# Optimization experiments

Hardware: AMD Instinct MI355X
Metric: run time of the kernel (lower is better)

Reference implementation:

```python
import jax, jax.numpy as jnp
import numpy as np

DIM = 768; DEPTH = 8; HEADS = 12; DH = 64; DFF = 2048
SOFTCLAMP = 50.0; TIME_EVERY = 4
B, T, S = 2, 32, 256
EPS = 1e-6


def rmsnorm(x, w):
    return x * jax.lax.rsqrt(jnp.mean(x * x, axis=-1, keepdims=True) + EPS) * w


def l2norm(x):
    n = jnp.sqrt(jnp.sum(x * x, axis=-1, keepdims=True))
    return x / jnp.maximum(n, 1e-12)


def make_rotary(n):
    inv = 1.0 / (10000.0 ** (jnp.arange(0, DH, 2, dtype=jnp.float32) / DH))
    f = jnp.arange(n, dtype=jnp.float32)[:, None] * inv[None, :]
    return jnp.concatenate([f, f], axis=-1)  # (n, DH)


def apply_rot(rot, x):
    # x: (B', H, n, DH), rot: (n, DH)
    x1, x2 = jnp.split(x, 2, axis=-1)
    return x * jnp.cos(rot) + jnp.concatenate([-x2, x1], axis=-1) * jnp.sin(rot)


def attn_block(x, rv, nw, wq, wk, wv, wo, wg, wmix, bm, kgam, rot, causal):
    # x: (B', n, DIM); rv: (B', H, n, DH) value-residual
    Bp, n, _ = x.shape
    tn = rmsnorm(x, nw)
    q = (tn @ wq).reshape(Bp, n, HEADS, DH).transpose(0, 2, 1, 3)
    k = (tn @ wk).reshape(Bp, n, HEADS, DH).transpose(0, 2, 1, 3)
    v = (tn @ wv).reshape(Bp, n, HEADS, DH).transpose(0, 2, 1, 3)
    # learned value-residual lerp: v <- v + mix * (rv - v)
    mix = jax.nn.sigmoid(tn @ wmix + bm).transpose(0, 2, 1)[..., None]
    v = v + mix * (rv - v)
    # MultiHeadRMSNorm on keys: l2norm * (gamma+1) * sqrt(DH)
    k = l2norm(k) * ((kgam + 1.0) * (DH ** 0.5))[:, None, :]
    if rot is not None:
        q = apply_rot(rot, q)
        k = apply_rot(rot, k)
    sim = jnp.einsum('bhid,bhjd->bhij', q, k) * (DH ** -0.5)
    sim = jnp.tanh(sim / SOFTCLAMP) * SOFTCLAMP
    if causal:
        cm = jnp.triu(jnp.ones((n, n), dtype=bool), 1)
        sim = jnp.where(cm, -jnp.finfo(sim.dtype).max, sim)
    attn = jax.nn.softmax(sim, axis=-1)
    o = jnp.einsum('bhij,bhjd->bhid', attn, v)
    gates = jax.nn.sigmoid(tn @ wg).transpose(0, 2, 1)[..., None]
    o = o * gates
    o = o.transpose(0, 2, 1, 3).reshape(Bp, n, HEADS * DH)
    return o @ wo


def ff_block(x, nw, win, bi, wout, bo):
    tn = rmsnorm(x, nw)
    h = tn @ win + bi
    a, g = jnp.split(h, 2, axis=-1)
    return (a * jax.nn.gelu(g, approximate=False)) @ wout + bo


def setup_inputs() -> dict:
    key = jax.random.key(0)
    ks = jax.random.split(key, 16)
    def rn(k, shape, scale=0.02):
        return jax.random.normal(k, shape, dtype=jnp.float32) * scale
    return {
        'tokens': jax.random.normal(ks[0], (B, T, S, DIM), dtype=jnp.float32),
        'attn_norm_w': jnp.ones((DEPTH, DIM), jnp.float32),
        'Wq': rn(ks[1], (DEPTH, DIM, HEADS * DH)),
        'Wk': rn(ks[2], (DEPTH, DIM, HEADS * DH)),
        'Wv': rn(ks[3], (DEPTH, DIM, HEADS * DH)),
        'Wo': rn(ks[4], (DEPTH, HEADS * DH, DIM)),
        'Wg': rn(ks[5], (DEPTH, DIM, HEADS)),
        'Wmix': rn(ks[6], (DEPTH, DIM, HEADS)),
        'bmix': jnp.zeros((DEPTH, HEADS), jnp.float32),
        'k_gamma': rn(ks[7], (DEPTH, HEADS, DH)),
        'ff_norm_w': jnp.ones((DEPTH, DIM), jnp.float32),
        'Win': rn(ks[8], (DEPTH, DIM, 2 * DFF)),
        'b_in': jnp.zeros((DEPTH, 2 * DFF), jnp.float32),
        'Wout': rn(ks[9], (DEPTH, DFF, DIM)),
        'b_out': jnp.zeros((DEPTH, DIM), jnp.float32),
        'vr_norm_w': jnp.ones((DIM,), jnp.float32),
        'vr_W': rn(ks[10], (DIM, HEADS * DH)),
        'final_norm_w': jnp.ones((DIM,), jnp.float32),
    }


def reference(tokens, attn_norm_w, Wq, Wk, Wv, Wo, Wg, Wmix, bmix, k_gamma,
              ff_norm_w, Win, b_in, Wout, b_out, vr_norm_w, vr_W, final_norm_w):
    b, t, s, d = tokens.shape
    # value residuals computed once from the input tokens
    rv = (rmsnorm(tokens, vr_norm_w) @ vr_W).reshape(b, t, s, HEADS, DH)
    rot = make_rotary(t)
    x = tokens
    for i in range(DEPTH):
        is_time = ((i + 1) % TIME_EVERY == 0)
        if is_time:
            xa = x.transpose(0, 2, 1, 3).reshape(b * s, t, d)
            rva = rv.transpose(0, 2, 3, 1, 4).reshape(b * s, HEADS, t, DH)
            o = attn_block(xa, rva, attn_norm_w[i], Wq[i], Wk[i], Wv[i], Wo[i],
                           Wg[i], Wmix[i], bmix[i], k_gamma[i], rot, True)
            o = o.reshape(b, s, t, d).transpose(0, 2, 1, 3)
        else:
            xa = x.reshape(b * t, s, d)
            rva = rv.transpose(0, 1, 3, 2, 4).reshape(b * t, HEADS, s, DH)
            o = attn_block(xa, rva, attn_norm_w[i], Wq[i], Wk[i], Wv[i], Wo[i],
                           Wg[i], Wmix[i], bmix[i], k_gamma[i], None, False)
            o = o.reshape(b, t, s, d)
        x = x + o
        x = x + ff_block(x, ff_norm_w[i], Win[i], b_in[i], Wout[i], b_out[i])
    return rmsnorm(x, final_norm_w)
```

## Files before the change

kernel.cpp:

```cpp
#include <hip/hip_runtime.h>
#include <cmath>

#define DIM 768
#define DEPTH 8
#define HEADS 12
#define DH 64
#define DFF 2048
#define NTOK 16384
#define BB 2
#define TT 32
#define SS 256
#define LDQ 2304

typedef __attribute__((ext_vector_type(8))) short short8;
typedef __attribute__((ext_vector_type(4))) float f32x4;

__device__ __forceinline__ float sigmoidf_(float x) { return 1.0f / (1.0f + __expf(-x)); }
__device__ __forceinline__ float geluf_(float x) {
  return 0.5f * x * (1.0f + erff(x * 0.70710678118654752f));
}
__device__ __forceinline__ unsigned short f2bf(float x) {
  union { float f; unsigned int u; } a; a.f = x;
  unsigned int r = a.u + 0x7fff + ((a.u >> 16) & 1);
  return (unsigned short)(r >> 16);
}
__device__ __forceinline__ float bf2f(unsigned short h) {
  union { unsigned int u; float f; } a; a.u = ((unsigned int)h) << 16;
  return a.f;
}
__device__ __forceinline__ void load_lds16(const void* g, void* l) {
  __builtin_amdgcn_global_load_lds(
      (const __attribute__((address_space(1))) unsigned int*)g,
      (__attribute__((address_space(3))) unsigned int*)l, 16, 0, 0);
}
__device__ __forceinline__ float softclamp_exp(float sv) {
  float a = exp2f(sv * 0.057707802f);
  float rc = __builtin_amdgcn_rcpf(a + 1.0f);
  return exp2f(fmaf(-144.26950408f, rc, 72.13475204f));
}

template<int BF>
__global__ __launch_bounds__(256) void rmsnorm_kernel(
    const float* __restrict__ x, const float* __restrict__ w, void* __restrict__ outp)
{
  int row = blockIdx.x;
  int tid = threadIdx.x;
  const float* xr = x + (size_t)row * DIM;
  float v0 = xr[tid], v1 = xr[tid + 256], v2 = xr[tid + 512];
  float ss = v0 * v0 + v1 * v1 + v2 * v2;
  #pragma unroll
  for (int off = 32; off; off >>= 1) ss += __shfl_xor(ss, off);
  __shared__ float sred[4];
  if ((tid & 63) == 0) sred[tid >> 6] = ss;
  __syncthreads();
  float tot = sred[0] + sred[1] + sred[2] + sred[3];
  float r = rsqrtf(tot * (1.0f / DIM) + 1e-6f);
  if (BF) {
    unsigned short* orow = (unsigned short*)outp + (size_t)row * DIM;
    orow[tid]       = f2bf(v0 * r * w[tid]);
    orow[tid + 256] = f2bf(v1 * r * w[tid + 256]);
    orow[tid + 512] = f2bf(v2 * r * w[tid + 512]);
  } else {
    float* orow = (float*)outp + (size_t)row * DIM;
    orow[tid]       = v0 * r * w[tid];
    orow[tid + 256] = v1 * r * w[tid + 256];
    orow[tid + 512] = v2 * r * w[tid + 512];
  }
}

__global__ __launch_bounds__(256) void w_to_bt(
    const float* __restrict__ W, unsigned short* __restrict__ WT, int K, int N)
{
  __shared__ float t[32][33];
  int n0 = blockIdx.x * 32, k0 = blockIdx.y * 32;
  int c = threadIdx.x & 31, r8 = threadIdx.x >> 5;
  #pragma unroll
  for (int rr = r8; rr < 32; rr += 8)
    t[rr][c] = W[(size_t)(k0 + rr) * N + n0 + c];
  __syncthreads();
  #pragma unroll
  for (int rn = r8; rn < 32; rn += 8)
    WT[(size_t)(n0 + rn) * K + k0 + c] = f2bf(t[c][rn]);
}

__global__ __launch_bounds__(256) void w_convert_layer(
    const float* __restrict__ Wq, const float* __restrict__ Wk,
    const float* __restrict__ Wv, const float* __restrict__ Wo,
    const float* __restrict__ Win, const float* __restrict__ Wout,
    unsigned short* __restrict__ wqkvT, unsigned short* __restrict__ woT,
    unsigned short* __restrict__ winT, unsigned short* __restrict__ woutT)
{
  __shared__ float tle[32][33];
  int t = blockIdx.x;
  const float* W; unsigned short* WT; int K, N, n0, k0, glu = 0;
  if (t < 1728) {
    int rg = t / 576, tt = t - rg * 576;
    W = (rg == 0) ? Wq : (rg == 1) ? Wk : Wv;
    WT = wqkvT + (size_t)rg * 768 * 768;
    K = 768; N = 768; n0 = (tt % 24) * 32; k0 = (tt / 24) * 32;
  } else if (t < 2304) {
    int tt = t - 1728; W = Wo; WT = woT;
    K = 768; N = 768; n0 = (tt % 24) * 32; k0 = (tt / 24) * 32;
  } else if (t < 5376) {
    int tt = t - 2304; W = Win; WT = winT;
    K = 768; N = 4096; n0 = (tt % 128) * 32; k0 = (tt / 128) * 32; glu = 1;
  } else {
    int tt = t - 5376; W = Wout; WT = woutT;
    K = 2048; N = 768; n0 = (tt % 24) * 32; k0 = (tt / 24) * 32;
  }
  int c = threadIdx.x & 31, r8 = threadIdx.x >> 5;
  int col = n0 + c;
  int scol = col;
  if (glu) {
    int b = col >> 5, rr2 = col & 31;
    scol = (rr2 < 16) ? (b * 16 + rr2) : (2048 + b * 16 + rr2 - 16);
  }
  for (int rr = r8; rr < 32; rr += 8)
    tle[rr][c] = W[(size_t)(k0 + rr) * N + scol];
  __syncthreads();
  for (int rn = r8; rn < 32; rn += 8)
    WT[(size_t)(n0 + rn) * K + k0 + c] = f2bf(tle[c][rn]);
}

template<int MODE>
__global__ __launch_bounds__(256) void gemm_bf16(
    const unsigned short* __restrict__ A, const unsigned short* __restrict__ BT,
    float* __restrict__ Cf, unsigned short* __restrict__ Hg,
    const float* __restrict__ bias, int M, int N, int K)
{
  __shared__ unsigned short As[128 * 32];
  __shared__ unsigned short Bs[128 * 32];
  const int tid = threadIdx.x;
  const int wave = tid >> 6;
  const int lane = tid & 63;
  const int bm = blockIdx.y * 128;
  const int bn = blockIdx.x * 128;
  const int wm = (wave & 1) * 64;
  const int wn = (wave >> 1) * 64;

  f32x4 acc[4][4];
  #pragma unroll
  for (int i = 0; i < 4; ++i)
    #pragma unroll
    for (int j = 0; j < 4; ++j) acc[i][j] = (f32x4){0.f, 0.f, 0.f, 0.f};

  const int srow = wave * 32 + (lane >> 2);
  const int skoff = (lane & 3) * 8;
  const unsigned short* gA = A + (size_t)(bm + srow) * K + skoff;
  const unsigned short* gB = BT + (size_t)(bn + srow) * K + skoff;
  unsigned short* lA = &As[(wave * 32) * 32];
  unsigned short* lB = &Bs[(wave * 32) * 32];

  const int fr = lane & 15;
  const int fq = (lane >> 4) * 8;

  for (int k0 = 0; k0 < K; k0 += 32) {
    load_lds16(gA + k0, lA);
    load_lds16(gA + k0 + 16 * K, lA + 16 * 32);
    load_lds16(gB + k0, lB);
    load_lds16(gB + k0 + 16 * K, lB + 16 * 32);
    __syncthreads();
    short8 a[4], b[4];
    #pragma unroll
    for (int i = 0; i < 4; ++i)
      a[i] = *(const short8*)&As[(wm + 16 * i + fr) * 32 + fq];
    #pragma unroll
    for (int j = 0; j < 4; ++j)
      b[j] = *(const short8*)&Bs[(wn + 16 * j + fr) * 32 + fq];
    #pragma unroll
    for (int i = 0; i < 4; ++i)
      #pragma unroll
      for (int j = 0; j < 4; ++j)
        acc[i][j] = __builtin_amdgcn_mfma_f32_16x16x32_bf16(a[i], b[j], acc[i][j], 0, 0, 0);
    __syncthreads();
  }

  const int crow0 = bm + wm + (lane >> 4) * 4;
  const int ccol0 = bn + wn + fr;
  float bv[4];
  if (MODE != 3) {
    #pragma unroll
    for (int j = 0; j < 4; ++j) bv[j] = bias ? bias[ccol0 + 16 * j] : 0.0f;
  }
  #pragma unroll
  for (int i = 0; i < 4; ++i) {
    #pragma unroll
    for (int r = 0; r < 4; ++r) {
      int row = crow0 + 16 * i + r;
      if (MODE == 3) {
        #pragma unroll
        for (int pj = 0; pj < 2; ++pj) {
          int b32 = (bn + wn + 32 * pj) >> 5;
          float av = acc[i][2 * pj][r] + bias[b32 * 16 + fr];
          float gv = acc[i][2 * pj + 1][r] + bias[2048 + b32 * 16 + fr];
          Hg[(size_t)row * (N >> 1) + b32 * 16 + fr] = f2bf(av * geluf_(gv));
        }
      } else {
        #pragma unroll
        for (int j = 0; j < 4; ++j) {
          int col = ccol0 + 16 * j;
          size_t idx = (size_t)row * N + col;
          float val = acc[i][j][r] + bv[j];
          if (MODE == 0) Cf[idx] = val;
          else if (MODE == 1) Cf[idx] += val;
          else Hg[idx] = f2bf(val);
        }
      }
    }
  }
}

__global__ __launch_bounds__(256) void proj12x2_kernel(
    const unsigned short* __restrict__ A, const float* __restrict__ Bw1,
    const float* __restrict__ b1, const float* __restrict__ Bw2,
    float* __restrict__ out1, float* __restrict__ out2)
{
  int row = blockIdx.x * 4 + (threadIdx.x >> 6);
  int lane = threadIdx.x & 63;
  const unsigned short* ar = A + (size_t)row * DIM;
  float acc1[HEADS], acc2[HEADS];
  #pragma unroll
  for (int j = 0; j < HEADS; ++j) { acc1[j] = 0.0f; acc2[j] = 0.0f; }
  for (int k2 = lane; k2 < DIM; k2 += 64) {
    float a = bf2f(ar[k2]);
    const float* bw1 = Bw1 + (size_t)k2 * HEADS;
    const float* bw2 = Bw2 + (size_t)k2 * HEADS;
    #pragma unroll
    for (int j = 0; j < HEADS; ++j) {
      acc1[j] = fmaf(a, bw1[j], acc1[j]);
      acc2[j] = fmaf(a, bw2[j], acc2[j]);
    }
  }
  #pragma unroll
  for (int j = 0; j < HEADS; ++j) {
    #pragma unroll
    for (int off = 32; off; off >>= 1) {
      acc1[j] += __shfl_xor(acc1[j], off);
      acc2[j] += __shfl_xor(acc2[j], off);
    }
  }
  if (lane < HEADS) {
    out1[(size_t)row * HEADS + lane] = sigmoidf_(acc1[lane] + b1[lane]);
    out2[(size_t)row * HEADS + lane] = sigmoidf_(acc2[lane]);
  }
}

__global__ __launch_bounds__(768) void qkv_fix_kernel(
    unsigned short* __restrict__ qkv, const unsigned short* __restrict__ rvb,
    const float* __restrict__ mix, const float* __restrict__ kgam, int is_time)
{
  int tok = blockIdx.x;
  int h = threadIdx.x >> 6;
  int d = threadIdx.x & 63;
  size_t rowb = (size_t)tok * LDQ + h * DH + d;
  float kv = bf2f(qkv[rowb + 768]);
  float ss = kv * kv;
  #pragma unroll
  for (int off = 32; off; off >>= 1) ss += __shfl_xor(ss, off);
  float nrm = fmaxf(sqrtf(ss), 1e-12f);
  kv = kv / nrm * (kgam[h * DH + d] + 1.0f) * 8.0f;
  float mv = mix[(size_t)tok * HEADS + h];
  float vv = bf2f(qkv[rowb + 1536]);
  float rvv = bf2f(rvb[(size_t)tok * DIM + h * DH + d]);
  qkv[rowb + 1536] = f2bf(vv + mv * (rvv - vv));
  float qv = bf2f(qkv[rowb]);
  if (is_time) {
    int t = (tok >> 8) & 31;
    int j = d & 31;
    float ang = (float)t * __expf(-(float)j * (9.210340371976184f / 32.0f));
    float cs = cosf(ang), sn = sinf(ang);
    float qp = __shfl_xor(qv, 32);
    float kp = __shfl_xor(kv, 32);
    float sgn = (d < 32) ? -1.0f : 1.0f;
    qv = qv * cs + sgn * qp * sn;
    kv = kv * cs + sgn * kp * sn;
  }
  qkv[rowb] = f2bf(qv);
  qkv[rowb + 768] = f2bf(kv);
}

__global__ __launch_bounds__(256, 2) void attn_mfma_kernel(
    const unsigned short* __restrict__ q, const unsigned short* __restrict__ k,
    const unsigned short* __restrict__ v, const unsigned short* __restrict__ rvb,
    const float* __restrict__ mix, const float* __restrict__ gate,
    const float* __restrict__ kgam, unsigned short* __restrict__ o)
{
  __shared__ __align__(16) unsigned short Ks[128 * 64];
  __shared__ __align__(16) unsigned short VsT[64 * 128];
  __shared__ __align__(16) unsigned short Pw[4][32 * 64];
  const int tid = threadIdx.x;
  const int wave = tid >> 6;
  const int lane = tid & 63;
  const int g = lane >> 4;
  const int c16 = lane & 15;
  const int bp = blockIdx.x >> 1;
  const int qh = blockIdx.x & 1;
  const int h = blockIdx.y;
  const size_t qoff = (size_t)bp * SS * LDQ + h * DH;
  const int qbase = qh * 128 + wave * 32;

  short8 aq[2][2];
  #pragma unroll
  for (int i = 0; i < 2; ++i) {
    const unsigned short* qp = q + qoff + (size_t)(qbase + i * 16 + c16) * LDQ;
    #pragma unroll
    for (int cc = 0; cc < 2; ++cc)
      aq[i][cc] = *(const short8*)(qp + cc * 32 + g * 8);
  }

  f32x4 oacc[2][4];
  float rs[2][4];
  #pragma unroll
  for (int i = 0; i < 2; ++i)
    #pragma unroll
    for (int j = 0; j < 4; ++j) {
      oacc[i][j] = (f32x4){0.f, 0.f, 0.f, 0.f};
      rs[i][j] = 0.f;
    }

  for (int half = 0; half < 2; ++half) {
    const int r0 = half * 128;
    #pragma unroll
    for (int it = 0; it < 4; ++it) {
      int f = tid + it * 256;
      int row = f >> 3, u = f & 7;
      short8 t8 = *(const short8*)(k + qoff + (size_t)(r0 + row) * LDQ + u * 8);
      float kv[8];
      float ss = 0.f;
      #pragma unroll
      for (int c = 0; c < 8; ++c) { kv[c] = bf2f((unsigned short)t8[c]); ss += kv[c] * kv[c]; }
      ss += __shfl_xor(ss, 1); ss += __shfl_xor(ss, 2); ss += __shfl_xor(ss, 4);
      float inv = 8.0f / fmaxf(sqrtf(ss), 1e-12f);
      float4 kg0 = *(const float4*)(kgam + h * DH + u * 8);
      float4 kg1 = *(const float4*)(kgam + h * DH + u * 8 + 4);
      short8 o8;
      o8[0] = (short)f2bf(kv[0] * inv * (kg0.x + 1.0f));
      o8[1] = (short)f2bf(kv[1] * inv * (kg0.y + 1.0f));
      o8[2] = (short)f2bf(kv[2] * inv * (kg0.z + 1.0f));
      o8[3] = (short)f2bf(kv[3] * inv * (kg0.w + 1.0f));
      o8[4] = (short)f2bf(kv[4] * inv * (kg1.x + 1.0f));
      o8[5] = (short)f2bf(kv[5] * inv * (kg1.y + 1.0f));
      o8[6] = (short)f2bf(kv[6] * inv * (kg1.z + 1.0f));
      o8[7] = (short)f2bf(kv[7] * inv * (kg1.w + 1.0f));
      *(short8*)&Ks[row * 64 + ((u ^ (row & 7)) << 3)] = o8;
    }
    #pragma unroll
    for (int it = 0; it < 4; ++it) {
      int f = tid + it * 256;
      int j = f & 127, dq = f >> 7;
      int tok = bp * SS + r0 + j;
      short8 v8 = *(const short8*)(v + qoff + (size_t)(r0 + j) * LDQ + dq * 8);
      short8 r8 = *(const short8*)(rvb + (size_t)tok * DIM + h * DH + dq * 8);
      float mv = mix[(size_t)tok * HEADS + h];
      int u = j >> 3;
      #pragma unroll
      for (int c = 0; c < 8; ++c) {
        int d = dq * 8 + c;
        float vv = bf2f((unsigned short)v8[c]);
        float val = vv + mv * (bf2f((unsigned short)r8[c]) - vv);
        VsT[d * 128 + ((u ^ (d & 15)) << 3) + (j & 7)] = f2bf(val);
      }
    }
    __syncthreads();

    #pragma unroll
    for (int jc = 0; jc < 2; ++jc) {
      const int lr0 = jc * 64;
      #pragma unroll
      for (int jh = 0; jh < 2; ++jh) {
        f32x4 s[2][2];
        #pragma unroll
        for (int i = 0; i < 2; ++i)
          #pragma unroll
          for (int j = 0; j < 2; ++j) s[i][j] = (f32x4){0.f, 0.f, 0.f, 0.f};
        #pragma unroll
        for (int j2 = 0; j2 < 2; ++j2) {
          int jt = jh * 2 + j2;
          int row = lr0 + jt * 16 + c16;
          short8 b0 = *(const short8*)&Ks[row * 64 + ((g ^ (row & 7)) << 3)];
          short8 b1 = *(const short8*)&Ks[row * 64 + (((4 + g) ^ (row & 7)) << 3)];
          #pragma unroll
          for (int i = 0; i < 2; ++i) {
            s[i][j2] = __builtin_amdgcn_mfma_f32_16x16x32_bf16(aq[i][0], b0, s[i][j2], 0, 0, 0);
            s[i][j2] = __builtin_amdgcn_mfma_f32_16x16x32_bf16(aq[i][1], b1, s[i][j2], 0, 0, 0);
          }
        }
        #pragma unroll
        for (int i = 0; i < 2; ++i) {
          #pragma unroll
          for (int j2 = 0; j2 < 2; ++j2) {
            int pj = (jh * 2 + j2) * 16 + c16;
            int uj = pj >> 3;
            #pragma unroll
            for (int r = 0; r < 4; ++r) {
              float p = softclamp_exp(s[i][j2][r] * 0.125f);
              unsigned short pb = f2bf(p);
              rs[i][r] += bf2f(pb);
              int prow = i * 16 + g * 4 + r;
              Pw[wave][prow * 64 + ((uj ^ (prow & 7)) << 3) + (pj & 7)] = pb;
            }
          }
        }
      }
      #pragma unroll
      for (int jj = 0; jj < 2; ++jj) {
        short8 pa[2];
        #pragma unroll
        for (int i = 0; i < 2; ++i) {
          int prow = i * 16 + c16;
          int u = jj * 4 + g;
          pa[i] = *(const short8*)&Pw[wave][prow * 64 + ((u ^ (prow & 7)) << 3)];
        }
        const int jl = lr0 + jj * 32 + g * 8;
        const int uv = jl >> 3;
        #pragma unroll
        for (int dt = 0; dt < 4; ++dt) {
          int d = dt * 16 + c16;
          short8 bv = *(const short8*)&VsT[d * 128 + ((uv ^ (d & 15)) << 3)];
          #pragma unroll
          for (int i = 0; i < 2; ++i)
            oacc[i][dt] = __builtin_amdgcn_mfma_f32_16x16x32_bf16(pa[i], bv, oacc[i][dt], 0, 0, 0);
        }
      }
    }
    __syncthreads();
  }

  #pragma unroll
  for (int i = 0; i < 2; ++i)
    #pragma unroll
    for (int r = 0; r < 4; ++r) {
      float t = rs[i][r];
      t += __shfl_xor(t, 1); t += __shfl_xor(t, 2);
      t += __shfl_xor(t, 4); t += __shfl_xor(t, 8);
      rs[i][r] = t;
    }
  #pragma unroll
  for (int i = 0; i < 2; ++i) {
    #pragma unroll
    for (int r = 0; r < 4; ++r) {
      int row = qbase + i * 16 + g * 4 + r;
      int tq = bp * SS + row;
      float gt = gate[(size_t)tq * HEADS + h] / rs[i][r];
      unsigned short* op = o + (size_t)tq * DIM + h * DH;
      #pragma unroll
      for (int dt = 0; dt < 4; ++dt)
        op[dt * 16 + c16] = f2bf(oacc[i][dt][r] * gt);
    }
  }
}

__global__ __launch_bounds__(256, 2) void attn_time_mfma(
    const unsigned short* __restrict__ q, const unsigned short* __restrict__ k,
    const unsigned short* __restrict__ v, const float* __restrict__ gate,
    unsigned short* __restrict__ o)
{
  __shared__ __align__(16) unsigned short VT[4][64 * 32];
  __shared__ __align__(16) unsigned short Pw[4][32 * 32];
  const int tid = threadIdx.x;
  const int wave = tid >> 6;
  const int lane = tid & 63;
  const int g = lane >> 4;
  const int c16 = lane & 15;
  const int h = blockIdx.y;
  const int sp = blockIdx.x * 4 + wave;
  const int base = (sp >> 8) * (TT * SS) + (sp & 255);

  short8 aq[2][2], bk[2][2];
  #pragma unroll
  for (int i = 0; i < 2; ++i) {
    const unsigned short* qp = q + (size_t)(base + (i * 16 + c16) * SS) * LDQ + h * DH;
    const unsigned short* kp = k + (size_t)(base + (i * 16 + c16) * SS) * LDQ + h * DH;
    #pragma unroll
    for (int cc = 0; cc < 2; ++cc) {
      aq[i][cc] = *(const short8*)(qp + cc * 32 + g * 8);
      bk[i][cc] = *(const short8*)(kp + cc * 32 + g * 8);
    }
  }

  {
    int tp = lane >> 1;
    int dh0 = (lane & 1) * 32;
    const unsigned short* vp = v + (size_t)(base + tp * SS) * LDQ + h * DH + dh0;
    int ut = tp >> 3;
    #pragma unroll
    for (int j4 = 0; j4 < 4; ++j4) {
      short8 t = *(const short8*)(vp + j4 * 8);
      #pragma unroll
      for (int c = 0; c < 8; ++c) {
        int d = dh0 + j4 * 8 + c;
        VT[wave][d * 32 + ((ut ^ (d & 3)) << 3) + (tp & 7)] = (unsigned short)t[c];
      }
    }
  }

  f32x4 s[2][2];
  #pragma unroll
  for (int i = 0; i < 2; ++i)
    #pragma unroll
    for (int j = 0; j < 2; ++j) s[i][j] = (f32x4){0.f, 0.f, 0.f, 0.f};
  #pragma unroll
  for (int jt = 0; jt < 2; ++jt)
    #pragma unroll
    for (int i = 0; i < 2; ++i) {
      s[i][jt] = __builtin_amdgcn_mfma_f32_16x16x32_bf16(aq[i][0], bk[jt][0], s[i][jt], 0, 0, 0);
      s[i][jt] = __builtin_amdgcn_mfma_f32_16x16x32_bf16(aq[i][1], bk[jt][1], s[i][jt], 0, 0, 0);
    }

  float rs[2][4];
  #pragma unroll
  for (int i = 0; i < 2; ++i)
    #pragma unroll
    for (int r = 0; r < 4; ++r) rs[i][r] = 0.f;
  #pragma unroll
  for (int i = 0; i < 2; ++i) {
    #pragma unroll
    for (int jt = 0; jt < 2; ++jt) {
      int pj = jt * 16 + c16;
      int uj = pj >> 3;
      #pragma unroll
      for (int r = 0; r < 4; ++r) {
        int t = i * 16 + g * 4 + r;
        float p = softclamp_exp(s[i][jt][r] * 0.125f);
        unsigned short pb = (pj <= t) ? f2bf(p) : (unsigned short)0;
        rs[i][r] += bf2f(pb);
        Pw[wave][t * 32 + ((uj ^ (t & 3)) << 3) + (pj & 7)] = pb;
      }
    }
  }

  short8 pa[2];
  #pragma unroll
  for (int i = 0; i < 2; ++i) {
    int prow = i * 16 + c16;
    pa[i] = *(const short8*)&Pw[wave][prow * 32 + ((g ^ (prow & 3)) << 3)];
  }
  f32x4 oacc[2][4];
  #pragma unroll
  for (int dt = 0; dt < 4; ++dt) {
    int d = dt * 16 + c16;
    short8 bv = *(const short8*)&VT[wave][d * 32 + ((g ^ (d & 3)) << 3)];
    #pragma unroll
    for (int i = 0; i < 2; ++i)
      oacc[i][dt] = __builtin_amdgcn_mfma_f32_16x16x32_bf16(
          pa[i], bv, (f32x4){0.f, 0.f, 0.f, 0.f}, 0, 0, 0);
  }

  #pragma unroll
  for (int i = 0; i < 2; ++i)
    #pragma unroll
    for (int r = 0; r < 4; ++r) {
      float t = rs[i][r];
      t += __shfl_xor(t, 1); t += __shfl_xor(t, 2);
      t += __shfl_xor(t, 4); t += __shfl_xor(t, 8);
      rs[i][r] = t;
    }
  #pragma unroll
  for (int i = 0; i < 2; ++i) {
    #pragma unroll
    for (int r = 0; r < 4; ++r) {
      int t = i * 16 + g * 4 + r;
      int tok = base + t * SS;
      float gt = gate[(size_t)tok * HEADS + h] / rs[i][r];
      unsigned short* op = o + (size_t)tok * DIM + h * DH;
      #pragma unroll
      for (int dt = 0; dt < 4; ++dt)
        op[dt * 16 + c16] = f2bf(oacc[i][dt][r] * gt);
    }
  }
}

extern "C" void kernel_launch(void* const* d_in, const int* in_sizes, int n_in,
                              void* d_out, int out_size, void* d_ws, size_t ws_size,
                              hipStream_t stream)
{
  const float* tokens = (const float*)d_in[0];
  const float* attn_norm_w = (const float*)d_in[1];
  const float* Wq   = (const float*)d_in[2];
  const float* Wk   = (const float*)d_in[3];
  const float* Wv   = (const float*)d_in[4];
  const float* Wo   = (const float*)d_in[5];
  const float* Wg   = (const float*)d_in[6];
  const float* Wmix = (const float*)d_in[7];
  const float* bmix = (const float*)d_in[8];
  const float* kgam = (const float*)d_in[9];
  const float* ffw  = (const float*)d_in[10];
  const float* Win  = (const float*)d_in[11];
  const float* bin  = (const float*)d_in[12];
  const float* Wout = (const float*)d_in[13];
  const float* bout = (const float*)d_in[14];
  const float* vrw  = (const float*)d_in[15];
  const float* vrW  = (const float*)d_in[16];
  const float* fnw  = (const float*)d_in[17];

  const size_t NT = (size_t)NTOK * DIM;
  float* ws  = (float*)d_ws;
  float* x   = ws;
  float* mix = x + NT;
  float* gate = mix + (size_t)NTOK * HEADS;
  unsigned short* tn   = (unsigned short*)(gate + (size_t)NTOK * HEADS);
  unsigned short* qkv  = tn + NT;
  unsigned short* rvb  = qkv + (size_t)NTOK * LDQ;
  unsigned short* wqkvT = rvb + NT;
  unsigned short* woT  = wqkvT + (size_t)2304 * 768;
  unsigned short* winT = woT + (size_t)768 * 768;
  unsigned short* woutT= winT + (size_t)4096 * 768;
  unsigned short* vrWT = woutT + (size_t)768 * 2048;
  unsigned short* hg   = qkv;

  hipMemcpyAsync(x, tokens, NT * sizeof(float), hipMemcpyDeviceToDevice, stream);

  w_to_bt<<<dim3(24, 24), 256, 0, stream>>>(vrW, vrWT, DIM, DIM);
  rmsnorm_kernel<1><<<NTOK, 256, 0, stream>>>(tokens, vrw, tn);
  gemm_bf16<2><<<dim3(6, 128), 256, 0, stream>>>(
      tn, vrWT, nullptr, rvb, nullptr, NTOK, DIM, DIM);

  for (int i = 0; i < DEPTH; ++i) {
    int is_time = ((i + 1) % 4 == 0) ? 1 : 0;
    w_convert_layer<<<6912, 256, 0, stream>>>(
        Wq + (size_t)i * DIM * DIM, Wk + (size_t)i * DIM * DIM,
        Wv + (size_t)i * DIM * DIM, Wo + (size_t)i * DIM * DIM,
        Win + (size_t)i * DIM * 2 * DFF, Wout + (size_t)i * DFF * DIM,
        wqkvT, woT, winT, woutT);

    rmsnorm_kernel<1><<<NTOK, 256, 0, stream>>>(x, attn_norm_w + (size_t)i * DIM, tn);
    gemm_bf16<2><<<dim3(18, 128), 256, 0, stream>>>(
        tn, wqkvT, nullptr, qkv, nullptr, NTOK, LDQ, DIM);
    proj12x2_kernel<<<NTOK / 4, 256, 0, stream>>>(
        tn, Wmix + (size_t)i * DIM * HEADS, bmix + (size_t)i * HEADS,
        Wg + (size_t)i * DIM * HEADS, mix, gate);
    if (is_time) {
      qkv_fix_kernel<<<dim3(NTOK), 768, 0, stream>>>(
          qkv, rvb, mix, kgam + (size_t)i * HEADS * DH, is_time);
      attn_time_mfma<<<dim3((BB * SS) / 4, HEADS), 256, 0, stream>>>(
          qkv, qkv + 768, qkv + 1536, gate, tn);
    } else {
      attn_mfma_kernel<<<dim3(BB * TT * 2, HEADS), 256, 0, stream>>>(
          qkv, qkv + 768, qkv + 1536, rvb, mix, gate,
          kgam + (size_t)i * HEADS * DH, tn);
    }
    gemm_bf16<1><<<dim3(6, 128), 256, 0, stream>>>(tn, woT, x, nullptr, nullptr, NTOK, DIM, DIM);
    rmsnorm_kernel<1><<<NTOK, 256, 0, stream>>>(x, ffw + (size_t)i * DIM, tn);
    gemm_bf16<3><<<dim3(32, 128), 256, 0, stream>>>(
        tn, winT, nullptr, hg, bin + (size_t)i * 2 * DFF, NTOK, 2 * DFF, DIM);
    gemm_bf16<1><<<dim3(6, 128), 256, 0, stream>>>(
        hg, woutT, x, nullptr, bout + (size_t)i * DIM, NTOK, DIM, DFF);
  }
  rmsnorm_kernel<0><<<NTOK, 256, 0, stream>>>(x, fnw, (float*)d_out);
}
```

Before: 4.495 ms.

## Double GEMM K-tile to 64 with XOR-swizzled LDS layout and fast erf GELU

The bf16 GEMM now stages a 64-wide K slice per iteration instead of 32, which halves the number of barriers per K loop. It stores tiles in LDS with an XOR swizzle on 16-byte chunks so the MFMA fragment reads avoid bank conflicts. Separately, the exact erff in GELU is replaced by the Abramowitz–Stegun polynomial approximation using rcp and exp, which lowers ALU cost in the FF epilogue at the price of a small accuracy loss. LDS use per block doubles, which may reduce occupancy.

Measured after the change: 4.429 ms. Within noise of the previous version (-1.5%).

```diff
diff --git a/kernel.cpp b/kernel.cpp
--- a/kernel.cpp
+++ b/kernel.cpp
@@ -17,7 +17,13 @@
 
 __device__ __forceinline__ float sigmoidf_(float x) { return 1.0f / (1.0f + __expf(-x)); }
 __device__ __forceinline__ float geluf_(float x) {
-  return 0.5f * x * (1.0f + erff(x * 0.70710678118654752f));
+  float z = fabsf(x) * 0.70710678118654752f;
+  float t = __builtin_amdgcn_rcpf(fmaf(0.3275911f, z, 1.0f));
+  float poly = t * fmaf(t, fmaf(t, fmaf(t, fmaf(t, 1.061405429f, -1.453152027f),
+                    1.421413741f), -0.284496736f), 0.254829592f);
+  float erfv = 1.0f - poly * __expf(-z * z);
+  erfv = copysignf(erfv, x);
+  return 0.5f * x * (1.0f + erfv);
 }
 __device__ __forceinline__ unsigned short f2bf(float x) {
   union { float f; unsigned int u; } a; a.f = x;
@@ -128,8 +134,8 @@
     float* __restrict__ Cf, unsigned short* __restrict__ Hg,
     const float* __restrict__ bias, int M, int N, int K)
 {
-  __shared__ unsigned short As[128 * 32];
-  __shared__ unsigned short Bs[128 * 32];
+  __shared__ unsigned short As[128 * 64];
+  __shared__ unsigned short Bs[128 * 64];
   const int tid = threadIdx.x;
   const int wave = tid >> 6;
   const int lane = tid & 63;
@@ -144,34 +150,42 @@
     #pragma unroll
     for (int j = 0; j < 4; ++j) acc[i][j] = (f32x4){0.f, 0.f, 0.f, 0.f};
 
-  const int srow = wave * 32 + (lane >> 2);
-  const int skoff = (lane & 3) * 8;
-  const unsigned short* gA = A + (size_t)(bm + srow) * K + skoff;
-  const unsigned short* gB = BT + (size_t)(bn + srow) * K + skoff;
-  unsigned short* lA = &As[(wave * 32) * 32];
-  unsigned short* lB = &Bs[(wave * 32) * 32];
+  const int srow = wave * 8 + (lane >> 3);
+  const int sku = ((lane & 7) ^ (lane >> 3)) * 8;
+  const unsigned short* gA = A + (size_t)(bm + srow) * K + sku;
+  const unsigned short* gB = BT + (size_t)(bn + srow) * K + sku;
+  unsigned short* lA = &As[wave * 512];
+  unsigned short* lB = &Bs[wave * 512];
 
   const int fr = lane & 15;
-  const int fq = (lane >> 4) * 8;
-
-  for (int k0 = 0; k0 < K; k0 += 32) {
-    load_lds16(gA + k0, lA);
-    load_lds16(gA + k0 + 16 * K, lA + 16 * 32);
-    load_lds16(gB + k0, lB);
-    load_lds16(gB + k0 + 16 * K, lB + 16 * 32);
+  const int fg = lane >> 4;
+
+  for (int k0 = 0; k0 < K; k0 += 64) {
+    #pragma unroll
+    for (int it = 0; it < 4; ++it) {
+      load_lds16(gA + k0 + (size_t)(it * 32) * K, lA + it * 2048);
+      load_lds16(gB + k0 + (size_t)(it * 32) * K, lB + it * 2048);
+    }
     __syncthreads();
-    short8 a[4], b[4];
-    #pragma unroll
-    for (int i = 0; i < 4; ++i)
-      a[i] = *(const short8*)&As[(wm + 16 * i + fr) * 32 + fq];
-    #pragma unroll
-    for (int j = 0; j < 4; ++j)
-      b[j] = *(const short8*)&Bs[(wn + 16 * j + fr) * 32 + fq];
-    #pragma unroll
-    for (int i = 0; i < 4; ++i)
-      #pragma unroll
-      for (int j = 0; j < 4; ++j)
-        acc[i][j] = __builtin_amdgcn_mfma_f32_16x16x32_bf16(a[i], b[j], acc[i][j], 0, 0, 0);
+    #pragma unroll
+    for (int s = 0; s < 2; ++s) {
+      short8 a[4], b[4];
+      #pragma unroll
+      for (int i = 0; i < 4; ++i) {
+        int row = wm + 16 * i + fr;
+        a[i] = *(const short8*)&As[row * 64 + (((s * 4 + fg) ^ (row & 7)) << 3)];
+      }
+      #pragma unroll
+      for (int j = 0; j < 4; ++j) {
+        int row = wn + 16 * j + fr;
+        b[j] = *(const short8*)&Bs[row * 64 + (((s * 4 + fg) ^ (row & 7)) << 3)];
+      }
+      #pragma unroll
+      for (int i = 0; i < 4; ++i)
+        #pragma unroll
+        for (int j = 0; j < 4; ++j)
+          acc[i][j] = __builtin_amdgcn_mfma_f32_16x16x32_bf16(a[i], b[j], acc[i][j], 0, 0, 0);
+    }
     __syncthreads();
   }
 
```
